# Kernel optimization log

Hardware: AMD Instinct MI355X
Metric: run time of the kernel (lower is better)

Reference implementation:

```python
import jax, jax.numpy as jnp
import numpy as np

N, E, CIN = 50000, 400000, 512
GH, GO, TH, HEADS, COUT = 128, 64, 64, 4, 32
BN_EPS = 1e-5


def setup_inputs() -> dict:
    key = jax.random.key(0)
    ks = jax.random.split(key, 40)
    i = iter(range(40))
    nrm = lambda shape, s=0.05: jax.random.normal(ks[next(i)], shape, jnp.float32) * s
    uni = lambda shape, lo, hi: jax.random.uniform(ks[next(i)], shape, jnp.float32, lo, hi)
    inp = {
        'x': jax.random.normal(ks[next(i)], (N, CIN), jnp.float32),
        'edge_index': jax.random.randint(ks[next(i)], (2, E), 0, N, jnp.int32),
        'edge_weight': uni((E,), 0.0, 1.0),
        # GCN layer 1 + BN1 (eval-mode running stats)
        'W1': nrm((CIN, GH)), 'b1': jnp.zeros((GH,), jnp.float32),
        'g1': uni((GH,), 0.9, 1.1), 'be1': nrm((GH,)), 'm1': nrm((GH,)), 'v1': uni((GH,), 0.5, 1.5),
        # GCN layer 2 + BN2
        'W2': nrm((GH, GO)), 'b2': jnp.zeros((GO,), jnp.float32),
        'g2': uni((GO,), 0.9, 1.1), 'be2': nrm((GO,)), 'm2': nrm((GO,)), 'v2': uni((GO,), 0.5, 1.5),
        # TransformerConv (PyG): lin_q/k/v: GO -> HEADS*TH ; skip: GO -> TH
        'Wq': nrm((GO, HEADS * TH)), 'bq': jnp.zeros((HEADS * TH,), jnp.float32),
        'Wk': nrm((GO, HEADS * TH)), 'bk': jnp.zeros((HEADS * TH,), jnp.float32),
        'Wv': nrm((GO, HEADS * TH)), 'bv': jnp.zeros((HEADS * TH,), jnp.float32),
        'Wskip': nrm((GO, TH)), 'bskip': jnp.zeros((TH,), jnp.float32),
        # BN after transformer
        'gt': uni((TH,), 0.9, 1.1), 'bet': nrm((TH,)), 'mt': nrm((TH,)), 'vt': uni((TH,), 0.5, 1.5),
        # final Linear
        'Wfc': nrm((TH, COUT)), 'bfc': jnp.zeros((COUT,), jnp.float32),
    }
    return inp


def _bn_eval(h, g, b, m, v):
    return (h - m) * (g / jnp.sqrt(v + BN_EPS)) + b


def _gcn_conv(x, src, dst, w, W, b):
    # add self loops with weight 1 (PyG gcn_norm default)
    loop = jnp.arange(N, dtype=src.dtype)
    s = jnp.concatenate([src, loop])
    d = jnp.concatenate([dst, loop])
    w2 = jnp.concatenate([w, jnp.ones((N,), x.dtype)])
    deg = jax.ops.segment_sum(w2, d, num_segments=N)
    dinv = jnp.where(deg > 0, jax.lax.rsqrt(deg), 0.0)
    norm = dinv[s] * w2 * dinv[d]                      # [E+N]
    h = x @ W                                          # [N, F]
    out = jax.ops.segment_sum(norm[:, None] * h[s], d, num_segments=N)
    return out + b


def _transformer_conv(x, src, dst, Wq, bq, Wk, bk, Wv, bv, Wskip, bskip):
    # PyG TransformerConv, concat=False (mean over heads), root_weight=True, no self loops
    q = (x @ Wq + bq).reshape(N, HEADS, TH)
    k = (x @ Wk + bk).reshape(N, HEADS, TH)
    v = (x @ Wv + bv).reshape(N, HEADS, TH)
    score = jnp.einsum('ehd,ehd->eh', q[dst], k[src]) / jnp.sqrt(jnp.float32(TH))  # [E,H]
    smax = jax.ops.segment_max(score, dst, num_segments=N)       # [N,H]
    ex = jnp.exp(score - smax[dst])
    denom = jax.ops.segment_sum(ex, dst, num_segments=N)         # [N,H]
    alpha = ex / (denom[dst] + 1e-16)                            # edge softmax over incoming edges
    agg = jax.ops.segment_sum(alpha[:, :, None] * v[src], dst, num_segments=N)  # [N,H,TH]
    out = agg.mean(axis=1)                                       # concat=False -> head mean
    return out + x @ Wskip + bskip


def reference(x, edge_index, edge_weight,
              W1, b1, g1, be1, m1, v1,
              W2, b2, g2, be2, m2, v2,
              Wq, bq, Wk, bk, Wv, bv, Wskip, bskip,
              gt, bet, mt, vt, Wfc, bfc):
    src, dst = edge_index[0], edge_index[1]
    h = _gcn_conv(x, src, dst, edge_weight, W1, b1)
    h = jax.nn.relu(_bn_eval(h, g1, be1, m1, v1))        # dropout = identity in eval
    h = _gcn_conv(h, src, dst, edge_weight, W2, b2)
    z = jax.nn.relu(_bn_eval(h, g2, be2, m2, v2))
    z = _transformer_conv(z, src, dst, Wq, bq, Wk, bk, Wv, bv, Wskip, bskip)
    z = jax.nn.relu(_bn_eval(z, gt, bet, mt, vt))
    return z @ Wfc + bfc
```

## Files before the change

### kernel.cpp

```cpp
#include <hip/hip_runtime.h>
#include <math.h>

namespace {

constexpr int NN = 50000;
constexpr int EE = 400000;
constexpr int CIN = 512;
constexpr int GH = 128;
constexpr int GO = 64;
constexpr int HEADS = 4;
constexpr int COUT = 32;
constexpr float EPS = 1e-5f;
constexpr int PBLK = (NN + 255) / 256;
constexpr int EDGEB = (EE + 255) / 256;
constexpr int CVTB = (NN * CIN) / 2048;
constexpr int PREPB = 128 + (79872 + 255) / 256;
constexpr int GM = (NN + 63) / 64;

typedef __attribute__((ext_vector_type(8))) _Float16 half8;
typedef __attribute__((ext_vector_type(4))) _Float16 half4;
typedef __attribute__((ext_vector_type(2))) _Float16 half2v;
typedef __attribute__((ext_vector_type(4))) float f32x4;

inline int cdiv(int a, int b) { return (a + b - 1) / b; }

__global__ void k_init0(float* deg, int* cnt) {
  int i = blockIdx.x * blockDim.x + threadIdx.x;
  if (i < NN) { deg[i] = 0.0f; cnt[i] = 0; }
}

__device__ __forceinline__ void prep_body(
    int b, int tid,
    const float* __restrict__ Wq, const float* __restrict__ Wk,
    const float* __restrict__ bq, const float* __restrict__ Wv,
    const float* __restrict__ bv, const float* __restrict__ bsk,
    const float* __restrict__ W1, const float* __restrict__ W2,
    const float* __restrict__ Wsk, const float* __restrict__ Wfc,
    _Float16* __restrict__ Mcp, float* __restrict__ cvec,
    _Float16* __restrict__ Bcatp, float* __restrict__ bcomb,
    _Float16* __restrict__ W1p, _Float16* __restrict__ W2p,
    _Float16* __restrict__ Wfcp) {
  if (b < 64) {
    const int i = b, col = tid, h = col >> 6, j = col & 63;
    float acc = 0.f;
    for (int t = 0; t < 64; ++t)
      acc += Wq[i * 256 + h * 64 + t] * Wk[j * 256 + h * 64 + t];
    Mcp[col * 64 + i] = (_Float16)(0.125f * acc);
    if (i == 0) {
      float c = 0.f;
      for (int t = 0; t < 64; ++t) c += bq[h * 64 + t] * Wk[j * 256 + h * 64 + t];
      cvec[col] = 0.125f * c;
    }
  } else if (b < 128) {
    const int idx = (b - 64) * 256 + tid;
    const int rr = idx >> 6, t = idx & 63;
    const int h = rr >> 6, c = rr & 63;
    Bcatp[(size_t)t * 320 + 64 + rr] = (_Float16)(0.25f * Wv[c * 256 + h * 64 + t]);
    if (b == 64 && tid < 64) {
      float s = 0.f;
#pragma unroll
      for (int h2 = 0; h2 < 4; ++h2) s += bv[h2 * 64 + tid];
      bcomb[tid] = bsk[tid] + 0.25f * s;
    }
  } else {
    const int i = (b - 128) * 256 + tid;
    if (i < 65536) { int k = i >> 7, f = i & 127; W1p[f * 512 + k] = (_Float16)W1[i]; }
    else if (i < 73728) { int rel = i - 65536; int k = rel >> 6, f = rel & 63; W2p[f * 128 + k] = (_Float16)W2[rel]; }
    else if (i < 77824) { int rel = i - 73728; int k = rel >> 6, f = rel & 63; Bcatp[f * 320 + k] = (_Float16)Wsk[rel]; }
    else if (i < 79872) { int rel = i - 77824; int k = rel >> 5, f = rel & 31; Wfcp[f * 64 + k] = (_Float16)Wfc[rel]; }
  }
}

__launch_bounds__(256) __global__
void k_edgeprep(const int* __restrict__ ei, const float* __restrict__ w,
                float* __restrict__ deg, int* __restrict__ cnt,
                int* __restrict__ rank, const float* __restrict__ x,
                _Float16* __restrict__ x16,
                const float* __restrict__ Wq, const float* __restrict__ Wk,
                const float* __restrict__ bq, const float* __restrict__ Wv,
                const float* __restrict__ bv, const float* __restrict__ bsk,
                const float* __restrict__ W1, const float* __restrict__ W2,
                const float* __restrict__ Wsk, const float* __restrict__ Wfc,
                _Float16* __restrict__ Mcp, float* __restrict__ cvec,
                _Float16* __restrict__ Bcatp, float* __restrict__ bcomb,
                _Float16* __restrict__ W1p, _Float16* __restrict__ W2p,
                _Float16* __restrict__ Wfcp) {
  if (blockIdx.x < EDGEB) {
    int e = blockIdx.x * 256 + threadIdx.x;
    if (e < EE) {
      int d = ei[EE + e];
      atomicAdd(&deg[d], w[e]);
      rank[e] = atomicAdd(&cnt[d], 1);
    }
  } else if (blockIdx.x < EDGEB + CVTB) {
    const int base = (blockIdx.x - EDGEB) * 2048 + threadIdx.x * 8;
    const float4 f0 = *reinterpret_cast<const float4*>(x + base);
    const float4 f1 = *reinterpret_cast<const float4*>(x + base + 4);
    half8 o;
    o[0] = (_Float16)f0.x; o[1] = (_Float16)f0.y;
    o[2] = (_Float16)f0.z; o[3] = (_Float16)f0.w;
    o[4] = (_Float16)f1.x; o[5] = (_Float16)f1.y;
    o[6] = (_Float16)f1.z; o[7] = (_Float16)f1.w;
    *reinterpret_cast<half8*>(x16 + base) = o;
  } else {
    prep_body(blockIdx.x - EDGEB - CVTB, threadIdx.x, Wq, Wk, bq, Wv, bv, bsk,
              W1, W2, Wsk, Wfc, Mcp, cvec, Bcatp, bcomb, W1p, W2p, Wfcp);
  }
}

__global__ void k_node1(const int* __restrict__ cnt, float* __restrict__ dinv,
                        int* __restrict__ part, int* __restrict__ bsum,
                        int* __restrict__ blkhist) {
  __shared__ int wsm[4];
  __shared__ int lh[64];
  const int tid = threadIdx.x, lane = tid & 63, wv = tid >> 6;
  const int i = blockIdx.x * 256 + tid;
  if (tid < 64) lh[tid] = 0;
  __syncthreads();
  int v = (i < NN) ? cnt[i] : 0;
  if (i < NN) {
    dinv[i] = rsqrtf(dinv[i] + 1.0f);
    atomicAdd(&lh[min(v, 63)], 1);
  }
  int x = v;
#pragma unroll
  for (int s = 1; s < 64; s <<= 1) {
    int t = __shfl_up(x, s);
    if (lane >= s) x += t;
  }
  if (lane == 63) wsm[wv] = x;
  __syncthreads();
  if (tid == 0) {
    int r = 0;
#pragma unroll
    for (int j = 0; j < 4; ++j) { int t = wsm[j]; wsm[j] = r; r += t; }
    bsum[blockIdx.x] = r;
  }
  __syncthreads();
  if (i < NN) part[i] = wsm[wv] + x - v;
  if (tid < 64) blkhist[blockIdx.x * 64 + tid] = lh[tid];
}

__launch_bounds__(256) __global__
void k_small(int* __restrict__ bsum, int* __restrict__ ro,
             const int* __restrict__ blkhist, int* __restrict__ blkoff) {
  __shared__ int wsm[4];
  __shared__ int qsum[4][64];
  const int tid = threadIdx.x, lane = tid & 63, wv = tid >> 6;
  {
    int v = (tid < PBLK) ? bsum[tid] : 0;
    int x = v;
#pragma unroll
    for (int s = 1; s < 64; s <<= 1) {
      int t = __shfl_up(x, s);
      if (lane >= s) x += t;
    }
    if (lane == 63) wsm[wv] = x;
    __syncthreads();
    if (tid == 0) {
      int r = 0;
#pragma unroll
      for (int j = 0; j < 4; ++j) { int t = wsm[j]; wsm[j] = r; r += t; }
      ro[NN] = r;
    }
    __syncthreads();
    if (tid < PBLK) bsum[tid] = wsm[wv] + x - v;
  }
  const int c0 = wv * 49, c1 = c0 + 49;
  {
    int qs = 0;
    int k = c0;
    for (; k + 4 <= c1; k += 4) {
      int a = blkhist[(k + 0) * 64 + lane];
      int b = blkhist[(k + 1) * 64 + lane];
      int c = blkhist[(k + 2) * 64 + lane];
      int d = blkhist[(k + 3) * 64 + lane];
      qs += (a + b) + (c + d);
    }
    for (; k < c1; ++k) qs += blkhist[k * 64 + lane];
    qsum[wv][lane] = qs;
  }
  __syncthreads();
  int tot = qsum[0][lane] + qsum[1][lane] + qsum[2][lane] + qsum[3][lane];
  int x = tot;
#pragma unroll
  for (int s = 1; s < 64; s <<= 1) {
    int t = __shfl_up(x, s);
    if (lane >= s) x += t;
  }
  int run = x - tot;
  for (int q = 0; q < wv; ++q) run += qsum[q][lane];
  int k = c0;
  for (; k + 4 <= c1; k += 4) {
    int a = blkhist[(k + 0) * 64 + lane];
    int b = blkhist[(k + 1) * 64 + lane];
    int c = blkhist[(k + 2) * 64 + lane];
    int d = blkhist[(k + 3) * 64 + lane];
    blkoff[(k + 0) * 64 + lane] = run;
    blkoff[(k + 1) * 64 + lane] = run + a;
    blkoff[(k + 2) * 64 + lane] = run + a + b;
    blkoff[(k + 3) * 64 + lane] = run + a + b + c;
    run += (a + b) + (c + d);
  }
  for (; k < c1; ++k) {
    int c = blkhist[k * 64 + lane];
    blkoff[k * 64 + lane] = run;
    run += c;
  }
}

__global__ void k_node2(const int* __restrict__ part, const int* __restrict__ bsum,
                        int* __restrict__ ro, const int* __restrict__ cnt,
                        const int* __restrict__ blkoff, int* __restrict__ perm) {
  __shared__ int lcur[64];
  const int tid = threadIdx.x;
  const int i = blockIdx.x * 256 + tid;
  if (tid < 64) lcur[tid] = 0;
  if (i < NN) ro[i] = part[i] + bsum[i >> 8];
  __syncthreads();
  if (i < NN) {
    int b = min(cnt[i], 63);
    int r = atomicAdd(&lcur[b], 1);
    perm[blkoff[blockIdx.x * 64 + b] + r] = i;
  }
}

template <int F, int K, int LDA, bool OUTF32>
__device__ __forceinline__
void hgemm_body(int bid, const _Float16* __restrict__ Av,
                const _Float16* __restrict__ Bp, const float* __restrict__ bias,
                void* __restrict__ Cv, int M) {
  constexpr int MI = 4;
  constexpr int NR = F / 64;
  constexpr int FW = F / 4;
  constexpr int NT = K / 64;

  __shared__ _Float16 Ah[64 * 64];

  const int tid = threadIdx.x;
  const int lane = tid & 63;
  const int wc = tid >> 6;
  const int l15 = lane & 15, lhi = lane >> 4;
  const int m0 = bid * 64;
  const int r = tid >> 2, ch = tid & 3;
  const int gr = min(m0 + r, M - 1);

  f32x4 acc[MI][NR];
#pragma unroll
  for (int mi = 0; mi < MI; ++mi)
#pragma unroll
    for (int ni = 0; ni < NR; ++ni) acc[mi][ni] = (f32x4)0.0f;

  half8 xhA0, xhA1, xhB0, xhB1;
  auto LOADA = [&](int kk) {
    const half8* src = reinterpret_cast<const half8*>(
        Av + (size_t)gr * LDA + kk + ch * 16);
    xhA0 = src[0]; xhA1 = src[1];
  };
  auto LOADB = [&](int kk) {
    const half8* src = reinterpret_cast<const half8*>(
        Av + (size_t)gr * LDA + kk + ch * 16);
    xhB0 = src[0]; xhB1 = src[1];
  };
  const int sbase = r * 128 + ch * 32;
  const int ssw = (r & 7) << 4;
  auto STOREA = [&]() {
    *reinterpret_cast<half8*>((char*)Ah + (sbase ^ ssw)) = xhA0;
    *reinterpret_cast<half8*>((char*)Ah + ((sbase + 16) ^ ssw)) = xhA1;
  };
  auto STOREB = [&]() {
    *reinterpret_cast<half8*>((char*)Ah + (sbase ^ ssw)) = xhB0;
    *reinterpret_cast<half8*>((char*)Ah + ((sbase + 16) ^ ssw)) = xhB1;
  };

  LOADA(0);
  if constexpr (NT > 1) LOADB(64);

#pragma unroll
  for (int t = 0; t < NT; ++t) {
    if ((t & 1) == 0) STOREA(); else STOREB();
    __syncthreads();
    if ((t & 1) == 0) {
      if (t + 2 < NT) LOADA((t + 2) * 64);
    } else {
      if (t + 2 < NT) LOADB((t + 2) * 64);
    }
    const int k0 = t * 64;
#pragma unroll
    for (int ks = 0; ks < 2; ++ks) {
      half8 ah[MI];
#pragma unroll
      for (int mi = 0; mi < MI; ++mi) {
        const int row = mi * 16 + l15;
        const int off = (row * 128 + (ks * 32 + lhi * 8) * 2) ^ ((row & 7) << 4);
        ah[mi] = *reinterpret_cast<const half8*>((const char*)Ah + off);
      }
#pragma unroll
      for (int ni = 0; ni < NR; ++ni) {
        const int col = wc * FW + ni * 16 + l15;
        const half8 bf = *reinterpret_cast<const half8*>(
            Bp + (size_t)col * K + k0 + ks * 32 + lhi * 8);
#pragma unroll
        for (int mi = 0; mi < MI; ++mi)
          acc[mi][ni] = __builtin_amdgcn_mfma_f32_16x16x32_f16(ah[mi], bf, acc[mi][ni], 0, 0, 0);
      }
    }
    __syncthreads();
  }

#pragma unroll
  for (int ni = 0; ni < NR; ++ni) {
    const int col = wc * FW + ni * 16 + l15;
    const float bvv = bias ? bias[col] : 0.0f;
#pragma unroll
    for (int mi = 0; mi < MI; ++mi) {
#pragma unroll
      for (int rr = 0; rr < 4; ++rr) {
        const int orow = m0 + mi * 16 + lhi * 4 + rr;
        if (orow < M) {
          float val = acc[mi][ni][rr] + bvv;
          if (OUTF32)
            ((float*)Cv)[(size_t)orow * F + col] = val;
          else
            ((_Float16*)Cv)[(size_t)orow * F + col] = (_Float16)val;
        }
      }
    }
  }
}

template <int F, int K, int LDA, bool OUTF32>
__launch_bounds__(256) __global__
void hgemm(const _Float16* __restrict__ Av, const _Float16* __restrict__ Bp,
           const float* __restrict__ bias, void* __restrict__ Cv, int M) {
  hgemm_body<F, K, LDA, OUTF32>(blockIdx.x, Av, Bp, bias, Cv, M);
}

__launch_bounds__(256) __global__
void k_fillgemm1(const int* __restrict__ ei, const float* __restrict__ w,
                 const float* __restrict__ dinv, const int* __restrict__ ro,
                 const int* __restrict__ rank, int2* __restrict__ csrp,
                 const _Float16* __restrict__ x16,
                 const _Float16* __restrict__ W1p, _Float16* __restrict__ h1f,
                 int M) {
  if (blockIdx.x < GM) {
    hgemm_body<128, 512, 512, false>(blockIdx.x, x16, W1p, nullptr, h1f, M);
  } else {
    int e = (blockIdx.x - GM) * 256 + threadIdx.x;
    if (e < EE) {
      int s = ei[e], d = ei[EE + e];
      int p = ro[d] + rank[e];
      int2 pk;
      pk.x = s;
      pk.y = __float_as_int(dinv[s] * w[e] * dinv[d]);
      csrp[p] = pk;
    }
  }
}

__launch_bounds__(256) __global__
void k_aggfc(const _Float16* __restrict__ zu, const _Float16* __restrict__ Bcatp,
             const float* __restrict__ bcomb, const _Float16* __restrict__ Wfcp,
             const float* __restrict__ bfc, float* __restrict__ out, int M,
             const float* __restrict__ gt, const float* __restrict__ bet,
             const float* __restrict__ mt, const float* __restrict__ vt) {
  __shared__ _Float16 Ah[64 * 64];
  __shared__ _Float16 Gs[64 * 64];

  const int tid = threadIdx.x;
  const int lane = tid & 63;
  const int wid = tid >> 6;
  const int l15 = lane & 15, lhi = lane >> 4;
  const int m0 = blockIdx.x * 64;
  const int r = tid >> 2, ch = tid & 3;
  const int gr = min(m0 + r, M - 1);

  f32x4 acc[4];
#pragma unroll
  for (int mi = 0; mi < 4; ++mi) acc[mi] = (f32x4)0.0f;

  half8 xhA0, xhA1, xhB0, xhB1;
  auto LOADA = [&](int kk) {
    const half8* src = reinterpret_cast<const half8*>(
        zu + (size_t)gr * 320 + kk + ch * 16);
    xhA0 = src[0]; xhA1 = src[1];
  };
  auto LOADB = [&](int kk) {
    const half8* src = reinterpret_cast<const half8*>(
        zu + (size_t)gr * 320 + kk + ch * 16);
    xhB0 = src[0]; xhB1 = src[1];
  };
  const int sbase = r * 128 + ch * 32;
  const int ssw = (r & 7) << 4;
  auto STOREA = [&]() {
    *reinterpret_cast<half8*>((char*)Ah + (sbase ^ ssw)) = xhA0;
    *reinterpret_cast<half8*>((char*)Ah + ((sbase + 16) ^ ssw)) = xhA1;
  };
  auto STOREB = [&]() {
    *reinterpret_cast<half8*>((char*)Ah + (sbase ^ ssw)) = xhB0;
    *reinterpret_cast<half8*>((char*)Ah + ((sbase + 16) ^ ssw)) = xhB1;
  };

  LOADA(0);
  LOADB(64);
#pragma unroll
  for (int t = 0; t < 5; ++t) {
    if ((t & 1) == 0) STOREA(); else STOREB();
    __syncthreads();
    if ((t & 1) == 0) {
      if (t + 2 < 5) LOADA((t + 2) * 64);
    } else {
      if (t + 2 < 5) LOADB((t + 2) * 64);
    }
    const int k0 = t * 64;
#pragma unroll
    for (int ks = 0; ks < 2; ++ks) {
      half8 ah[4];
#pragma unroll
      for (int mi = 0; mi < 4; ++mi) {
        const int row = mi * 16 + l15;
        const int off = (row * 128 + (ks * 32 + lhi * 8) * 2) ^ ((row & 7) << 4);
        ah[mi] = *reinterpret_cast<const half8*>((const char*)Ah + off);
      }
      const int col = wid * 16 + l15;
      const half8 bf = *reinterpret_cast<const half8*>(
          Bcatp + (size_t)col * 320 + k0 + ks * 32 + lhi * 8);
#pragma unroll
      for (int mi = 0; mi < 4; ++mi)
        acc[mi] = __builtin_amdgcn_mfma_f32_16x16x32_f16(ah[mi], bf, acc[mi], 0, 0, 0);
    }
    __syncthreads();
  }

  {
    const int col = wid * 16 + l15;
    const float bns = gt[col] * rsqrtf(vt[col] + EPS);
    const float bnb = bet[col], bnm = mt[col], bco = bcomb[col];
#pragma unroll
    for (int mi = 0; mi < 4; ++mi) {
#pragma unroll
      for (int rr = 0; rr < 4; ++rr) {
        const int row = mi * 16 + lhi * 4 + rr;
        float val = acc[mi][rr] + bco;
        val = (val - bnm) * bns + bnb;
        val = val > 0.f ? val : 0.f;
        const int boff = (row * 128 + col * 2) ^ ((row & 7) << 4);
        *reinterpret_cast<_Float16*>((char*)Gs + boff) = (_Float16)val;
      }
    }
  }
  __syncthreads();

  f32x4 acc2[2];
#pragma unroll
  for (int ni = 0; ni < 2; ++ni) acc2[ni] = (f32x4)0.0f;
#pragma unroll
  for (int ks = 0; ks < 2; ++ks) {
    const int row = wid * 16 + l15;
    const int off = (row * 128 + (ks * 32 + lhi * 8) * 2) ^ ((row & 7) << 4);
    const half8 ag = *reinterpret_cast<const half8*>((const char*)Gs + off);
#pragma unroll
    for (int ni = 0; ni < 2; ++ni) {
      const int col = ni * 16 + l15;
      const half8 bf = *reinterpret_cast<const half8*>(
          Wfcp + (size_t)col * 64 + ks * 32 + lhi * 8);
      acc2[ni] = __builtin_amdgcn_mfma_f32_16x16x32_f16(ag, bf, acc2[ni], 0, 0, 0);
    }
  }
#pragma unroll
  for (int ni = 0; ni < 2; ++ni) {
    const int col = ni * 16 + l15;
#pragma unroll
    for (int rr = 0; rr < 4; ++rr) {
      const int orow = m0 + wid * 16 + lhi * 4 + rr;
      if (orow < M) out[(size_t)orow * COUT + col] = acc2[ni][rr] + bfc[col];
    }
  }
}

__launch_bounds__(256) __global__
void k_gcn128(const int* __restrict__ ro, const int2* __restrict__ csrp,
              const int* __restrict__ perm,
              const _Float16* __restrict__ h, const float* __restrict__ dinv,
              const float* __restrict__ bias, const float* __restrict__ g,
              const float* __restrict__ be, const float* __restrict__ m,
              const float* __restrict__ v, _Float16* __restrict__ out) {
  const int idx = blockIdx.x * 4 + (threadIdx.x >> 6);
  const int lane = threadIdx.x & 63;
  if (idx >= NN) return;
  const int wid = perm[idx];
  const float di = dinv[wid];
  const float di2 = di * di;
  const int p0 = ro[wid], p1 = ro[wid + 1];

  half2v sv = *reinterpret_cast<const half2v*>(h + (size_t)wid * 128 + lane * 2);
  float2 a[4];
  a[0] = make_float2((float)sv[0] * di2, (float)sv[1] * di2);
  a[1] = make_float2(0.f, 0.f);
  a[2] = make_float2(0.f, 0.f);
  a[3] = make_float2(0.f, 0.f);
  int p = p0;
  for (; p + 8 <= p1; p += 8) {
    int2 pk[8];
#pragma unroll
    for (int j = 0; j < 8; ++j) pk[j] = csrp[p + j];
    half2v hv[8];
#pragma unroll
    for (int j = 0; j < 8; ++j)
      hv[j] = *reinterpret_cast<const half2v*>(h + (size_t)pk[j].x * 128 + lane * 2);
#pragma unroll
    for (int j = 0; j < 8; ++j) {
      float w = __int_as_float(pk[j].y);
      a[j & 3].x += w * (float)hv[j][0];
      a[j & 3].y += w * (float)hv[j][1];
    }
  }
  for (; p + 4 <= p1; p += 4) {
    int2 pk[4];
#pragma unroll
    for (int j = 0; j < 4; ++j) pk[j] = csrp[p + j];
    half2v hv[4];
#pragma unroll
    for (int j = 0; j < 4; ++j)
      hv[j] = *reinterpret_cast<const half2v*>(h + (size_t)pk[j].x * 128 + lane * 2);
#pragma unroll
    for (int j = 0; j < 4; ++j) {
      float w = __int_as_float(pk[j].y);
      a[j].x += w * (float)hv[j][0];
      a[j].y += w * (float)hv[j][1];
    }
  }
  for (; p < p1; ++p) {
    int2 pk = csrp[p];
    float w = __int_as_float(pk.y);
    half2v hv = *reinterpret_cast<const half2v*>(h + (size_t)pk.x * 128 + lane * 2);
    a[1].x += w * (float)hv[0]; a[1].y += w * (float)hv[1];
  }
  float ax = (a[0].x + a[1].x) + (a[2].x + a[3].x);
  float ay = (a[0].y + a[1].y) + (a[2].y + a[3].y);
  float2 gg = reinterpret_cast<const float2*>(g)[lane];
  float2 bb = reinterpret_cast<const float2*>(be)[lane];
  float2 mm = reinterpret_cast<const float2*>(m)[lane];
  float2 vv = reinterpret_cast<const float2*>(v)[lane];
  float2 bi = reinterpret_cast<const float2*>(bias)[lane];
  float s0 = gg.x * rsqrtf(vv.x + EPS);
  float s1 = gg.y * rsqrtf(vv.y + EPS);
  float y0 = (ax + bi.x - mm.x) * s0 + bb.x;
  float y1 = (ay + bi.y - mm.y) * s1 + bb.y;
  half2v o;
  o[0] = (_Float16)(y0 > 0.f ? y0 : 0.f);
  o[1] = (_Float16)(y1 > 0.f ? y1 : 0.f);
  *reinterpret_cast<half2v*>(out + (size_t)wid * 128 + lane * 2) = o;
}

__launch_bounds__(256) __global__
void k_gcn64(const int* __restrict__ ro, const int2* __restrict__ csrp,
             const int* __restrict__ perm,
             const _Float16* __restrict__ h, const float* __restrict__ dinv,
             const float* __restrict__ bias, const float* __restrict__ g,
             const float* __restrict__ be, const float* __restrict__ m,
             const float* __restrict__ v, _Float16* __restrict__ zu) {
  const int idx = blockIdx.x * 4 + (threadIdx.x >> 6);
  const int lane = threadIdx.x & 63;
  if (idx >= NN) return;
  const int wid = perm[idx];
  const float di = dinv[wid];
  const float di2 = di * di;
  const int p0 = ro[wid], p1 = ro[wid + 1];

  float a[4];
  a[0] = (float)h[(size_t)wid * 64 + lane] * di2;
  a[1] = 0.f; a[2] = 0.f; a[3] = 0.f;
  int p = p0;
  for (; p + 8 <= p1; p += 8) {
    int2 pk[8];
#pragma unroll
    for (int j = 0; j < 8; ++j) pk[j] = csrp[p + j];
    float hv[8];
#pragma unroll
    for (int j = 0; j < 8; ++j) hv[j] = (float)h[(size_t)pk[j].x * 64 + lane];
#pragma unroll
    for (int j = 0; j < 8; ++j) a[j & 3] += __int_as_float(pk[j].y) * hv[j];
  }
  for (; p + 4 <= p1; p += 4) {
    int2 pk[4];
#pragma unroll
    for (int j = 0; j < 4; ++j) pk[j] = csrp[p + j];
    float hv[4];
#pragma unroll
    for (int j = 0; j < 4; ++j) hv[j] = (float)h[(size_t)pk[j].x * 64 + lane];
#pragma unroll
    for (int j = 0; j < 4; ++j) a[j] += __int_as_float(pk[j].y) * hv[j];
  }
  for (; p < p1; ++p) {
    int2 pk = csrp[p];
    a[1] += __int_as_float(pk.y) * (float)h[(size_t)pk.x * 64 + lane];
  }
  float av = (a[0] + a[1]) + (a[2] + a[3]);
  float sc = g[lane] * rsqrtf(v[lane] + EPS);
  float y = (av + bias[lane] - m[lane]) * sc + be[lane];
  zu[(size_t)wid * 320 + lane] = (_Float16)(y > 0.f ? y : 0.f);
}

__launch_bounds__(256) __global__
void k_attn(const int* __restrict__ ro, const int2* __restrict__ csrp,
            const int* __restrict__ perm, _Float16* zu,
            const _Float16* __restrict__ qpp) {
  const int wave = blockIdx.x * 4 + (threadIdx.x >> 6);
  const int lane = threadIdx.x & 63;
  const int g = lane >> 4;
  const int t = lane & 15;
  const bool bit3 = (t & 8) != 0, bit2 = (t & 4) != 0;

  const int idx = wave * 4 + g;
  const bool valid = idx < NN;
  const int dst = perm[valid ? idx : 0];

  float4 q[4];
#pragma unroll
  for (int h = 0; h < 4; ++h) {
    half4 qh = *reinterpret_cast<const half4*>(qpp + (size_t)dst * 256 + h * 64 + t * 4);
    q[h] = make_float4((float)qh[0], (float)qh[1], (float)qh[2], (float)qh[3]);
  }

  float4 ua[4];
  float den[4];
#pragma unroll
  for (int h = 0; h < 4; ++h) {
    ua[h] = make_float4(0.f, 0.f, 0.f, 0.f);
    den[h] = 0.f;
  }

  int p = valid ? ro[dst] : 0;
  const int pend = valid ? ro[dst + 1] : 0;

  auto reduce4 = [&](float pa0, float pa1, float pa2, float pa3,
                     float& o0, float& o1, float& o2, float& o3) {
    float send1 = bit3 ? pa0 : pa2;
    float recv1 = __shfl_xor(send1, 8);
    float a0 = (bit3 ? pa2 : pa0) + recv1;
    float send2 = bit3 ? pa1 : pa3;
    float recv2 = __shfl_xor(send2, 8);
    float a1 = (bit3 ? pa3 : pa1) + recv2;
    float send3 = bit2 ? a0 : a1;
    float recv3 = __shfl_xor(send3, 4);
    float b = (bit2 ? a1 : a0) + recv3;
    b += __shfl_xor(b, 2);
    b += __shfl_xor(b, 1);
    float r4 = __shfl_xor(b, 4);
    float r8 = __shfl_xor(b, 8);
    float r84 = __shfl_xor(r4, 8);
    o0 = bit3 ? (bit2 ? r84 : r8) : (bit2 ? r4 : b);
    o1 = bit3 ? (bit2 ? r8 : r84) : (bit2 ? b : r4);
    o2 = bit3 ? (bit2 ? r4 : b) : (bit2 ? r84 : r8);
    o3 = bit3 ? (bit2 ? b : r4) : (bit2 ? r8 : r84);
  };

  int sA = csrp[min(p, EE - 1)].x;
  int sB = csrp[min(p + 1, EE - 1)].x;
  half4 znA = *reinterpret_cast<const half4*>(zu + (size_t)sA * 320 + t * 4);
  half4 znB = *reinterpret_cast<const half4*>(zu + (size_t)sB * 320 + t * 4);

  while (__ballot(p < pend)) {
    const bool actA = p < pend;
    const bool actB = (p + 1) < pend;
    const float4 zvA = make_float4((float)znA[0], (float)znA[1], (float)znA[2], (float)znA[3]);
    const float4 zvB = make_float4((float)znB[0], (float)znB[1], (float)znB[2], (float)znB[3]);
    sA = csrp[min(p + 2, EE - 1)].x;
    sB = csrp[min(p + 3, EE - 1)].x;
    znA = *reinterpret_cast<const half4*>(zu + (size_t)sA * 320 + t * 4);
    znB = *reinterpret_cast<const half4*>(zu + (size_t)sB * 320 + t * 4);

    float pA0 = q[0].x * zvA.x + q[0].y * zvA.y + q[0].z * zvA.z + q[0].w * zvA.w;
    float pA1 = q[1].x * zvA.x + q[1].y * zvA.y + q[1].z * zvA.z + q[1].w * zvA.w;
    float pA2 = q[2].x * zvA.x + q[2].y * zvA.y + q[2].z * zvA.z + q[2].w * zvA.w;
    float pA3 = q[3].x * zvA.x + q[3].y * zvA.y + q[3].z * zvA.z + q[3].w * zvA.w;
    float pB0 = q[0].x * zvB.x + q[0].y * zvB.y + q[0].z * zvB.z + q[0].w * zvB.w;
    float pB1 = q[1].x * zvB.x + q[1].y * zvB.y + q[1].z * zvB.z + q[1].w * zvB.w;
    float pB2 = q[2].x * zvB.x + q[2].y * zvB.y + q[2].z * zvB.z + q[2].w * zvB.w;
    float pB3 = q[3].x * zvB.x + q[3].y * zvB.y + q[3].z * zvB.z + q[3].w * zvB.w;

    float sA0, sA1, sA2, sA3, sB0, sB1, sB2, sB3;
    reduce4(pA0, pA1, pA2, pA3, sA0, sA1, sA2, sA3);
    reduce4(pB0, pB1, pB2, pB3, sB0, sB1, sB2, sB3);

    float eA0 = actA ? __expf(fminf(sA0, 60.f)) : 0.f;
    float eA1 = actA ? __expf(fminf(sA1, 60.f)) : 0.f;
    float eA2 = actA ? __expf(fminf(sA2, 60.f)) : 0.f;
    float eA3 = actA ? __expf(fminf(sA3, 60.f)) : 0.f;
    float eB0 = actB ? __expf(fminf(sB0, 60.f)) : 0.f;
    float eB1 = actB ? __expf(fminf(sB1, 60.f)) : 0.f;
    float eB2 = actB ? __expf(fminf(sB2, 60.f)) : 0.f;
    float eB3 = actB ? __expf(fminf(sB3, 60.f)) : 0.f;

    den[0] += eA0 + eB0; den[1] += eA1 + eB1;
    den[2] += eA2 + eB2; den[3] += eA3 + eB3;
    ua[0].x += eA0 * zvA.x + eB0 * zvB.x; ua[0].y += eA0 * zvA.y + eB0 * zvB.y;
    ua[0].z += eA0 * zvA.z + eB0 * zvB.z; ua[0].w += eA0 * zvA.w + eB0 * zvB.w;
    ua[1].x += eA1 * zvA.x + eB1 * zvB.x; ua[1].y += eA1 * zvA.y + eB1 * zvB.y;
    ua[1].z += eA1 * zvA.z + eB1 * zvB.z; ua[1].w += eA1 * zvA.w + eB1 * zvB.w;
    ua[2].x += eA2 * zvA.x + eB2 * zvB.x; ua[2].y += eA2 * zvA.y + eB2 * zvB.y;
    ua[2].z += eA2 * zvA.z + eB2 * zvB.z; ua[2].w += eA2 * zvA.w + eB2 * zvB.w;
    ua[3].x += eA3 * zvA.x + eB3 * zvB.x; ua[3].y += eA3 * zvA.y + eB3 * zvB.y;
    ua[3].z += eA3 * zvA.z + eB3 * zvB.z; ua[3].w += eA3 * zvA.w + eB3 * zvB.w;
    p += 2;
  }

  if (valid) {
#pragma unroll
    for (int h = 0; h < 4; ++h) {
      float inv = 1.0f / (den[h] + 1e-16f);
      half4 o;
      o[0] = (_Float16)(ua[h].x * inv);
      o[1] = (_Float16)(ua[h].y * inv);
      o[2] = (_Float16)(ua[h].z * inv);
      o[3] = (_Float16)(ua[h].w * inv);
      *reinterpret_cast<half4*>(zu + (size_t)dst * 320 + 64 + h * 64 + t * 4) = o;
    }
  }
}

}

extern "C" void kernel_launch(void* const* d_in, const int* in_sizes, int n_in,
                              void* d_out, int out_size, void* d_ws, size_t ws_size,
                              hipStream_t stream) {
  const float* x   = (const float*)d_in[0];
  const int*   ei  = (const int*)d_in[1];
  const float* ew  = (const float*)d_in[2];
  const float* W1  = (const float*)d_in[3];
  const float* b1  = (const float*)d_in[4];
  const float* g1  = (const float*)d_in[5];
  const float* be1 = (const float*)d_in[6];
  const float* m1  = (const float*)d_in[7];
  const float* v1  = (const float*)d_in[8];
  const float* W2  = (const float*)d_in[9];
  const float* b2  = (const float*)d_in[10];
  const float* g2  = (const float*)d_in[11];
  const float* be2 = (const float*)d_in[12];
  const float* m2  = (const float*)d_in[13];
  const float* v2  = (const float*)d_in[14];
  const float* Wq  = (const float*)d_in[15];
  const float* bq  = (const float*)d_in[16];
  const float* Wk  = (const float*)d_in[17];
  const float* Wv  = (const float*)d_in[19];
  const float* bv  = (const float*)d_in[20];
  const float* Wsk = (const float*)d_in[21];
  const float* bsk = (const float*)d_in[22];
  const float* gt  = (const float*)d_in[23];
  const float* bet = (const float*)d_in[24];
  const float* mt  = (const float*)d_in[25];
  const float* vt  = (const float*)d_in[26];
  const float* Wfc = (const float*)d_in[27];
  const float* bfc = (const float*)d_in[28];

  constexpr int NP = 50048;
  float* ws = (float*)d_ws;
  float* dinv    = ws;
  int*   cnt     = (int*)(dinv + NP);
  int*   rank    = cnt + NP;
  int*   ro      = rank + EE;
  int*   perm    = ro + NP;
  int*   part    = perm + NP;
  int*   bsum    = part + NP;
  int2*  csrp    = (int2*)(bsum + 256);
  int*   blkhist = (int*)(csrp + EE);
  int*   blkoff  = blkhist + PBLK * 64;
  float* cvec    = (float*)(blkoff + PBLK * 64 + 64);
  float* bcomb   = cvec + 256;
  _Float16* Mcp   = (_Float16*)(bcomb + 64);
  _Float16* Bcatp = Mcp + 256 * 64;
  _Float16* W1p   = Bcatp + 64 * 320;
  _Float16* W2p   = W1p + 128 * 512;
  _Float16* Wfcp  = W2p + 64 * 128;
  _Float16* x16   = Wfcp + 32 * 64;
  _Float16* h1f   = x16 + (size_t)NP * 512;
  _Float16* a1f   = h1f + (size_t)NP * 128;
  _Float16* h2f   = a1f + (size_t)NP * 128;
  _Float16* zuf   = h2f + (size_t)NP * 64;
  _Float16* qppf  = zuf + (size_t)NP * 320;

  const int tb = 256;

  k_init0<<<cdiv(NN, tb), tb, 0, stream>>>(dinv, cnt);
  k_edgeprep<<<EDGEB + CVTB + PREPB, 256, 0, stream>>>(
      ei, ew, dinv, cnt, rank, x, x16, Wq, Wk, bq, Wv, bv, bsk, W1, W2, Wsk, Wfc,
      Mcp, cvec, Bcatp, bcomb, W1p, W2p, Wfcp);
  k_node1<<<PBLK, 256, 0, stream>>>(cnt, dinv, part, bsum, blkhist);
  k_small<<<1, 256, 0, stream>>>(bsum, ro, blkhist, blkoff);
  k_node2<<<PBLK, 256, 0, stream>>>(part, bsum, ro, cnt, blkoff, perm);

  k_fillgemm1<<<GM + EDGEB, 256, 0, stream>>>(ei, ew, dinv, ro, rank, csrp,
                                              x16, W1p, h1f, NN);

  k_gcn128<<<cdiv(NN, 4), 256, 0, stream>>>(ro, csrp, perm, h1f, dinv,
                                            b1, g1, be1, m1, v1, a1f);
  hgemm<64, 128, 128, false><<<GM, 256, 0, stream>>>(a1f, W2p, nullptr, h2f, NN);
  k_gcn64<<<cdiv(NN, 4), 256, 0, stream>>>(ro, csrp, perm, h2f, dinv,
                                           b2, g2, be2, m2, v2, zuf);

  hgemm<256, 64, 320, false><<<GM, 256, 0, stream>>>(zuf, Mcp, cvec, qppf, NN);
  k_attn<<<cdiv(NN, 16), 256, 0, stream>>>(ro, csrp, perm, zuf, qppf);

  k_aggfc<<<GM, 256, 0, stream>>>(zuf, Bcatp, bcomb, Wfcp, bfc, (float*)d_out, NN,
                                  gt, bet, mt, vt);
}
```

Before: 239.3 us.

## Fuse fp32-to-fp16 conversion into GEMM1 and compute degree from CSR

Removes the separate x→fp16 conversion pass: the first GEMM now loads fp32 x directly and converts it while staging into shared memory. This avoids writing and rereading the 51 MB fp16 copy, at the cost of doubled A-operand load bytes inside the GEMM. The atomic float degree accumulation is replaced by a new per-node kernel that sums CSR edge weights. The CSR now stores raw weights, so the GCN kernels gather dinv[src] per edge and scale by dinv[dst] at the end, adding an extra gather per edge.

```diff
diff --git a/kernel.cpp b/kernel.cpp
--- a/kernel.cpp
+++ b/kernel.cpp
@@ -13,7 +13,6 @@
 constexpr float EPS = 1e-5f;
 constexpr int PBLK = (NN + 255) / 256;
 constexpr int EDGEB = (EE + 255) / 256;
-constexpr int CVTB = (NN * CIN) / 2048;
 constexpr int PREPB = 128 + (79872 + 255) / 256;
 constexpr int GM = (NN + 63) / 64;
 
@@ -24,9 +23,9 @@
 
 inline int cdiv(int a, int b) { return (a + b - 1) / b; }
 
-__global__ void k_init0(float* deg, int* cnt) {
+__global__ void k_init0(int* cnt) {
   int i = blockIdx.x * blockDim.x + threadIdx.x;
-  if (i < NN) { deg[i] = 0.0f; cnt[i] = 0; }
+  if (i < NN) cnt[i] = 0;
 }
 
 __device__ __forceinline__ void prep_body(
@@ -72,10 +71,8 @@
 }
 
 __launch_bounds__(256) __global__
-void k_edgeprep(const int* __restrict__ ei, const float* __restrict__ w,
-                float* __restrict__ deg, int* __restrict__ cnt,
-                int* __restrict__ rank, const float* __restrict__ x,
-                _Float16* __restrict__ x16,
+void k_edgeprep(const int* __restrict__ ei, int* __restrict__ cnt,
+                int* __restrict__ rank,
                 const float* __restrict__ Wq, const float* __restrict__ Wk,
                 const float* __restrict__ bq, const float* __restrict__ Wv,
                 const float* __restrict__ bv, const float* __restrict__ bsk,
@@ -89,28 +86,16 @@
     int e = blockIdx.x * 256 + threadIdx.x;
     if (e < EE) {
       int d = ei[EE + e];
-      atomicAdd(&deg[d], w[e]);
       rank[e] = atomicAdd(&cnt[d], 1);
     }
-  } else if (blockIdx.x < EDGEB + CVTB) {
-    const int base = (blockIdx.x - EDGEB) * 2048 + threadIdx.x * 8;
-    const float4 f0 = *reinterpret_cast<const float4*>(x + base);
-    const float4 f1 = *reinterpret_cast<const float4*>(x + base + 4);
-    half8 o;
-    o[0] = (_Float16)f0.x; o[1] = (_Float16)f0.y;
-    o[2] = (_Float16)f0.z; o[3] = (_Float16)f0.w;
-    o[4] = (_Float16)f1.x; o[5] = (_Float16)f1.y;
-    o[6] = (_Float16)f1.z; o[7] = (_Float16)f1.w;
-    *reinterpret_cast<half8*>(x16 + base) = o;
   } else {
-    prep_body(blockIdx.x - EDGEB - CVTB, threadIdx.x, Wq, Wk, bq, Wv, bv, bsk,
+    prep_body(blockIdx.x - EDGEB, threadIdx.x, Wq, Wk, bq, Wv, bv, bsk,
               W1, W2, Wsk, Wfc, Mcp, cvec, Bcatp, bcomb, W1p, W2p, Wfcp);
   }
 }
 
-__global__ void k_node1(const int* __restrict__ cnt, float* __restrict__ dinv,
-                        int* __restrict__ part, int* __restrict__ bsum,
-                        int* __restrict__ blkhist) {
+__global__ void k_node1(const int* __restrict__ cnt, int* __restrict__ part,
+                        int* __restrict__ bsum, int* __restrict__ blkhist) {
   __shared__ int wsm[4];
   __shared__ int lh[64];
   const int tid = threadIdx.x, lane = tid & 63, wv = tid >> 6;
@@ -118,10 +103,7 @@
   if (tid < 64) lh[tid] = 0;
   __syncthreads();
   int v = (i < NN) ? cnt[i] : 0;
-  if (i < NN) {
-    dinv[i] = rsqrtf(dinv[i] + 1.0f);
-    atomicAdd(&lh[min(v, 63)], 1);
-  }
+  if (i < NN) atomicAdd(&lh[min(v, 63)], 1);
   int x = v;
 #pragma unroll
   for (int s = 1; s < 64; s <<= 1) {
@@ -225,9 +207,9 @@
   }
 }
 
-template <int F, int K, int LDA, bool OUTF32>
+template <int F, int K, int LDA, bool AF32C, bool OUTF32>
 __device__ __forceinline__
-void hgemm_body(int bid, const _Float16* __restrict__ Av,
+void hgemm_body(int bid, const void* __restrict__ Av,
                 const _Float16* __restrict__ Bp, const float* __restrict__ bias,
                 void* __restrict__ Cv, int M) {
   constexpr int MI = 4;
@@ -251,26 +233,69 @@
 #pragma unroll
     for (int ni = 0; ni < NR; ++ni) acc[mi][ni] = (f32x4)0.0f;
 
+  float xfA[16], xfB[16];
   half8 xhA0, xhA1, xhB0, xhB1;
+
   auto LOADA = [&](int kk) {
-    const half8* src = reinterpret_cast<const half8*>(
-        Av + (size_t)gr * LDA + kk + ch * 16);
-    xhA0 = src[0]; xhA1 = src[1];
+    if constexpr (AF32C) {
+      const float4* src = reinterpret_cast<const float4*>(
+          (const float*)Av + (size_t)gr * LDA + kk + ch * 16);
+      float4 f0 = src[0], f1 = src[1], f2 = src[2], f3 = src[3];
+      xfA[0] = f0.x; xfA[1] = f0.y; xfA[2] = f0.z; xfA[3] = f0.w;
+      xfA[4] = f1.x; xfA[5] = f1.y; xfA[6] = f1.z; xfA[7] = f1.w;
+      xfA[8] = f2.x; xfA[9] = f2.y; xfA[10] = f2.z; xfA[11] = f2.w;
+      xfA[12] = f3.x; xfA[13] = f3.y; xfA[14] = f3.z; xfA[15] = f3.w;
+    } else {
+      const half8* src = reinterpret_cast<const half8*>(
+          (const _Float16*)Av + (size_t)gr * LDA + kk + ch * 16);
+      xhA0 = src[0]; xhA1 = src[1];
+    }
   };
   auto LOADB = [&](int kk) {
-    const half8* src = reinterpret_cast<const half8*>(
-        Av + (size_t)gr * LDA + kk + ch * 16);
-    xhB0 = src[0]; xhB1 = src[1];
+    if constexpr (AF32C) {
+      const float4* src = reinterpret_cast<const float4*>(
+          (const float*)Av + (size_t)gr * LDA + kk + ch * 16);
+      float4 f0 = src[0], f1 = src[1], f2 = src[2], f3 = src[3];
+      xfB[0] = f0.x; xfB[1] = f0.y; xfB[2] = f0.z; xfB[3] = f0.w;
+      xfB[4] = f1.x; xfB[5] = f1.y; xfB[6] = f1.z; xfB[7] = f1.w;
+      xfB[8] = f2.x; xfB[9] = f2.y; xfB[10] = f2.z; xfB[11] = f2.w;
+      xfB[12] = f3.x; xfB[13] = f3.y; xfB[14] = f3.z; xfB[15] = f3.w;
+    } else {
+      const half8* src = reinterpret_cast<const half8*>(
+          (const _Float16*)Av + (size_t)gr * LDA + kk + ch * 16);
+      xhB0 = src[0]; xhB1 = src[1];
+    }
   };
+
   const int sbase = r * 128 + ch * 32;
   const int ssw = (r & 7) << 4;
   auto STOREA = [&]() {
-    *reinterpret_cast<half8*>((char*)Ah + (sbase ^ ssw)) = xhA0;
-    *reinterpret_cast<half8*>((char*)Ah + ((sbase + 16) ^ ssw)) = xhA1;
+    if constexpr (AF32C) {
+      half8 v0, v1;
+#pragma unroll
+      for (int i = 0; i < 8; ++i) v0[i] = (_Float16)xfA[i];
+#pragma unroll
+      for (int i = 0; i < 8; ++i) v1[i] = (_Float16)xfA[8 + i];
+      *reinterpret_cast<half8*>((char*)Ah + (sbase ^ ssw)) = v0;
+      *reinterpret_cast<half8*>((char*)Ah + ((sbase + 16) ^ ssw)) = v1;
+    } else {
+      *reinterpret_cast<half8*>((char*)Ah + (sbase ^ ssw)) = xhA0;
+      *reinterpret_cast<half8*>((char*)Ah + ((sbase + 16) ^ ssw)) = xhA1;
+    }
   };
   auto STOREB = [&]() {
-    *reinterpret_cast<half8*>((char*)Ah + (sbase ^ ssw)) = xhB0;
-    *reinterpret_cast<half8*>((char*)Ah + ((sbase + 16) ^ ssw)) = xhB1;
+    if constexpr (AF32C) {
+      half8 v0, v1;
+#pragma unroll
+      for (int i = 0; i < 8; ++i) v0[i] = (_Float16)xfB[i];
+#pragma unroll
+      for (int i = 0; i < 8; ++i) v1[i] = (_Float16)xfB[8 + i];
+      *reinterpret_cast<half8*>((char*)Ah + (sbase ^ ssw)) = v0;
+      *reinterpret_cast<half8*>((char*)Ah + ((sbase + 16) ^ ssw)) = v1;
+    } else {
+      *reinterpret_cast<half8*>((char*)Ah + (sbase ^ ssw)) = xhB0;
+      *reinterpret_cast<half8*>((char*)Ah + ((sbase + 16) ^ ssw)) = xhB1;
+    }
   };
 
   LOADA(0);
@@ -329,33 +354,48 @@
   }
 }
 
-template <int F, int K, int LDA, bool OUTF32>
+template <int F, int K, int LDA, bool AF32C, bool OUTF32>
 __launch_bounds__(256) __global__
-void hgemm(const _Float16* __restrict__ Av, const _Float16* __restrict__ Bp,
+void hgemm(const void* __restrict__ Av, const _Float16* __restrict__ Bp,
            const float* __restrict__ bias, void* __restrict__ Cv, int M) {
-  hgemm_body<F, K, LDA, OUTF32>(blockIdx.x, Av, Bp, bias, Cv, M);
+  hgemm_body<F, K, LDA, AF32C, OUTF32>(blockIdx.x, Av, Bp, bias, Cv, M);
 }
 
 __launch_bounds__(256) __global__
 void k_fillgemm1(const int* __restrict__ ei, const float* __restrict__ w,
-                 const float* __restrict__ dinv, const int* __restrict__ ro,
-                 const int* __restrict__ rank, int2* __restrict__ csrp,
-                 const _Float16* __restrict__ x16,
+                 const int* __restrict__ ro, const int* __restrict__ rank,
+                 int2* __restrict__ csrp, const float* __restrict__ x,
                  const _Float16* __restrict__ W1p, _Float16* __restrict__ h1f,
                  int M) {
   if (blockIdx.x < GM) {
-    hgemm_body<128, 512, 512, false>(blockIdx.x, x16, W1p, nullptr, h1f, M);
+    hgemm_body<128, 512, 512, true, false>(blockIdx.x, x, W1p, nullptr, h1f, M);
   } else {
     int e = (blockIdx.x - GM) * 256 + threadIdx.x;
     if (e < EE) {
-      int s = ei[e], d = ei[EE + e];
+      int d = ei[EE + e];
       int p = ro[d] + rank[e];
       int2 pk;
-      pk.x = s;
-      pk.y = __float_as_int(dinv[s] * w[e] * dinv[d]);
+      pk.x = ei[e];
+      pk.y = __float_as_int(w[e]);
       csrp[p] = pk;
     }
   }
+}
+
+__global__ void k_deg(const int* __restrict__ ro, const int2* __restrict__ csrp,
+                      float* __restrict__ dinv) {
+  int d = blockIdx.x * 256 + threadIdx.x;
+  if (d >= NN) return;
+  int p = ro[d];
+  const int p1 = ro[d + 1];
+  float s0 = 0.f, s1 = 0.f, s2 = 0.f, s3 = 0.f;
+  for (; p + 4 <= p1; p += 4) {
+    int2 a = csrp[p], b = csrp[p + 1], c = csrp[p + 2], e = csrp[p + 3];
+    s0 += __int_as_float(a.y); s1 += __int_as_float(b.y);
+    s2 += __int_as_float(c.y); s3 += __int_as_float(e.y);
+  }
+  for (; p < p1; ++p) s0 += __int_as_float(csrp[p].y);
+  dinv[d] = rsqrtf(1.0f + (s0 + s1) + (s2 + s3));
 }
 
 __launch_bounds__(256) __global__
@@ -480,22 +520,21 @@
 
 __launch_bounds__(256) __global__
 void k_gcn128(const int* __restrict__ ro, const int2* __restrict__ csrp,
-              const int* __restrict__ perm,
-              const _Float16* __restrict__ h, const float* __restrict__ dinv,
-              const float* __restrict__ bias, const float* __restrict__ g,
-              const float* __restrict__ be, const float* __restrict__ m,
-              const float* __restrict__ v, _Float16* __restrict__ out) {
+              const int* __restrict__ perm, const _Float16* __restrict__ h,
+              const float* __restrict__ dinv, const float* __restrict__ bias,
+              const float* __restrict__ g, const float* __restrict__ be,
+              const float* __restrict__ m, const float* __restrict__ v,
+              _Float16* __restrict__ out) {
   const int idx = blockIdx.x * 4 + (threadIdx.x >> 6);
   const int lane = threadIdx.x & 63;
   if (idx >= NN) return;
   const int wid = perm[idx];
   const float di = dinv[wid];
-  const float di2 = di * di;
   const int p0 = ro[wid], p1 = ro[wid + 1];
 
   half2v sv = *reinterpret_cast<const half2v*>(h + (size_t)wid * 128 + lane * 2);
   float2 a[4];
-  a[0] = make_float2((float)sv[0] * di2, (float)sv[1] * di2);
+  a[0] = make_float2((float)sv[0] * di, (float)sv[1] * di);
   a[1] = make_float2(0.f, 0.f);
   a[2] = make_float2(0.f, 0.f);
   a[3] = make_float2(0.f, 0.f);
@@ -504,40 +543,46 @@
     int2 pk[8];
 #pragma unroll
     for (int j = 0; j < 8; ++j) pk[j] = csrp[p + j];
+    float ds[8];
+#pragma unroll
+    for (int j = 0; j < 8; ++j) ds[j] = dinv[pk[j].x];
     half2v hv[8];
 #pragma unroll
     for (int j = 0; j < 8; ++j)
       hv[j] = *reinterpret_cast<const half2v*>(h + (size_t)pk[j].x * 128 + lane * 2);
 #pragma unroll
     for (int j = 0; j < 8; ++j) {
-      float w = __int_as_float(pk[j].y);
-      a[j & 3].x += w * (float)hv[j][0];
-      a[j & 3].y += w * (float)hv[j][1];
+      float c = ds[j] * __int_as_float(pk[j].y);
+      a[j & 3].x += c * (float)hv[j][0];
+      a[j & 3].y += c * (float)hv[j][1];
     }
   }
   for (; p + 4 <= p1; p += 4) {
     int2 pk[4];
 #pragma unroll
     for (int j = 0; j < 4; ++j) pk[j] = csrp[p + j];
+    float ds[4];
+#pragma unroll
+    for (int j = 0; j < 4; ++j) ds[j] = dinv[pk[j].x];
     half2v hv[4];
 #pragma unroll
     for (int j = 0; j < 4; ++j)
       hv[j] = *reinterpret_cast<const half2v*>(h + (size_t)pk[j].x * 128 + lane * 2);
 #pragma unroll
     for (int j = 0; j < 4; ++j) {
-      float w = __int_as_float(pk[j].y);
-      a[j].x += w * (float)hv[j][0];
-      a[j].y += w * (float)hv[j][1];
+      float c = ds[j] * __int_as_float(pk[j].y);
+      a[j].x += c * (float)hv[j][0];
+      a[j].y += c * (float)hv[j][1];
     }
   }
   for (; p < p1; ++p) {
     int2 pk = csrp[p];
-    float w = __int_as_float(pk.y);
+    float c = dinv[pk.x] * __int_as_float(pk.y);
     half2v hv = *reinterpret_cast<const half2v*>(h + (size_t)pk.x * 128 + lane * 2);
-    a[1].x += w * (float)hv[0]; a[1].y += w * (float)hv[1];
-  }
-  float ax = (a[0].x + a[1].x) + (a[2].x + a[3].x);
-  float ay = (a[0].y + a[1].y) + (a[2].y + a[3].y);
+    a[1].x += c * (float)hv[0]; a[1].y += c * (float)hv[1];
+  }
+  float ax = ((a[0].x + a[1].x) + (a[2].x + a[3].x)) * di;
+  float ay = ((a[0].y + a[1].y) + (a[2].y + a[3].y)) * di;
   float2 gg = reinterpret_cast<const float2*>(g)[lane];
   float2 bb = reinterpret_cast<const float2*>(be)[lane];
   float2 mm = reinterpret_cast<const float2*>(m)[lane];
@@ -555,48 +600,53 @@
 
 __launch_bounds__(256) __global__
 void k_gcn64(const int* __restrict__ ro, const int2* __restrict__ csrp,
-             const int* __restrict__ perm,
-             const _Float16* __restrict__ h, const float* __restrict__ dinv,
-             const float* __restrict__ bias, const float* __restrict__ g,
-             const float* __restrict__ be, const float* __restrict__ m,
-             const float* __restrict__ v, _Float16* __restrict__ zu) {
+             const int* __restrict__ perm, const _Float16* __restrict__ h,
+             const float* __restrict__ dinv, const float* __restrict__ bias,
+             const float* __restrict__ g, const float* __restrict__ be,
+             const float* __restrict__ m, const float* __restrict__ v,
+             _Float16* __restrict__ zu) {
   const int idx = blockIdx.x * 4 + (threadIdx.x >> 6);
   const int lane = threadIdx.x & 63;
   if (idx >= NN) return;
   const int wid = perm[idx];
   const float di = dinv[wid];
-  const float di2 = di * di;
   const int p0 = ro[wid], p1 = ro[wid + 1];
 
   float a[4];
-  a[0] = (float)h[(size_t)wid * 64 + lane] * di2;
+  a[0] = (float)h[(size_t)wid * 64 + lane] * di;
   a[1] = 0.f; a[2] = 0.f; a[3] = 0.f;
   int p = p0;
   for (; p + 8 <= p1; p += 8) {
     int2 pk[8];
 #pragma unroll
     for (int j = 0; j < 8; ++j) pk[j] = csrp[p + j];
+    float ds[8];
+#pragma unroll
+    for (int j = 0; j < 8; ++j) ds[j] = dinv[pk[j].x];
     float hv[8];
 #pragma unroll
     for (int j = 0; j < 8; ++j) hv[j] = (float)h[(size_t)pk[j].x * 64 + lane];
 #pragma unroll
-    for (int j = 0; j < 8; ++j) a[j & 3] += __int_as_float(pk[j].y) * hv[j];
+    for (int j = 0; j < 8; ++j) a[j & 3] += ds[j] * __int_as_float(pk[j].y) * hv[j];
   }
   for (; p + 4 <= p1; p += 4) {
     int2 pk[4];
 #pragma unroll
     for (int j = 0; j < 4; ++j) pk[j] = csrp[p + j];
+    float ds[4];
+#pragma unroll
+    for (int j = 0; j < 4; ++j) ds[j] = dinv[pk[j].x];
     float hv[4];
 #pragma unroll
     for (int j = 0; j < 4; ++j) hv[j] = (float)h[(size_t)pk[j].x * 64 + lane];
 #pragma unroll
-    for (int j = 0; j < 4; ++j) a[j] += __int_as_float(pk[j].y) * hv[j];
+    for (int j = 0; j < 4; ++j) a[j] += ds[j] * __int_as_float(pk[j].y) * hv[j];
   }
   for (; p < p1; ++p) {
     int2 pk = csrp[p];
-    a[1] += __int_as_float(pk.y) * (float)h[(size_t)pk.x * 64 + lane];
-  }
-  float av = (a[0] + a[1]) + (a[2] + a[3]);
+    a[1] += dinv[pk.x] * __int_as_float(pk.y) * (float)h[(size_t)pk.x * 64 + lane];
+  }
+  float av = ((a[0] + a[1]) + (a[2] + a[3])) * di;
   float sc = g[lane] * rsqrtf(v[lane] + EPS);
   float y = (av + bias[lane] - m[lane]) * sc + be[lane];
   zu[(size_t)wid * 320 + lane] = (_Float16)(y > 0.f ? y : 0.f);
@@ -773,8 +823,7 @@
   _Float16* W1p   = Bcatp + 64 * 320;
   _Float16* W2p   = W1p + 128 * 512;
   _Float16* Wfcp  = W2p + 64 * 128;
-  _Float16* x16   = Wfcp + 32 * 64;
-  _Float16* h1f   = x16 + (size_t)NP * 512;
+  _Float16* h1f   = Wfcp + 32 * 64;
   _Float16* a1f   = h1f + (size_t)NP * 128;
   _Float16* h2f   = a1f + (size_t)NP * 128;
   _Float16* zuf   = h2f + (size_t)NP * 64;
@@ -782,24 +831,25 @@
 
   const int tb = 256;
 
-  k_init0<<<cdiv(NN, tb), tb, 0, stream>>>(dinv, cnt);
-  k_edgeprep<<<EDGEB + CVTB + PREPB, 256, 0, stream>>>(
-      ei, ew, dinv, cnt, rank, x, x16, Wq, Wk, bq, Wv, bv, bsk, W1, W2, Wsk, Wfc,
+  k_init0<<<cdiv(NN, tb), tb, 0, stream>>>(cnt);
+  k_edgeprep<<<EDGEB + PREPB, 256, 0, stream>>>(
+      ei, cnt, rank, Wq, Wk, bq, Wv, bv, bsk, W1, W2, Wsk, Wfc,
       Mcp, cvec, Bcatp, bcomb, W1p, W2p, Wfcp);
-  k_node1<<<PBLK, 256, 0, stream>>>(cnt, dinv, part, bsum, blkhist);
+  k_node1<<<PBLK, 256, 0, stream>>>(cnt, part, bsum, blkhist);
   k_small<<<1, 256, 0, stream>>>(bsum, ro, blkhist, blkoff);
   k_node2<<<PBLK, 256, 0, stream>>>(part, bsum, ro, cnt, blkoff, perm);
 
-  k_fillgemm1<<<GM + EDGEB, 256, 0, stream>>>(ei, ew, dinv, ro, rank, csrp,
-                                              x16, W1p, h1f, NN);
+  k_fillgemm1<<<GM + EDGEB, 256, 0, stream>>>(ei, ew, ro, rank, csrp,
+                                              x, W1p, h1f, NN);
+  k_deg<<<cdiv(NN, tb), tb, 0, stream>>>(ro, csrp, dinv);
 
   k_gcn128<<<cdiv(NN, 4), 256, 0, stream>>>(ro, csrp, perm, h1f, dinv,
                                             b1, g1, be1, m1, v1, a1f);
-  hgemm<64, 128, 128, false><<<GM, 256, 0, stream>>>(a1f, W2p, nullptr, h2f, NN);
+  hgemm<64, 128, 128, false, false><<<GM, 256, 0, stream>>>(a1f, W2p, nullptr, h2f, NN);
   k_gcn64<<<cdiv(NN, 4), 256, 0, stream>>>(ro, csrp, perm, h2f, dinv,
                                            b2, g2, be2, m2, v2, zuf);
 
-  hgemm<256, 64, 320, false><<<GM, 256, 0, stream>>>(zuf, Mcp, cvec, qppf, NN);
+  hgemm<256, 64, 320, false, false><<<GM, 256, 0, stream>>>(zuf, Mcp, cvec, qppf, NN);
   k_attn<<<cdiv(NN, 16), 256, 0, stream>>>(ro, csrp, perm, zuf, qppf);
 
   k_aggfc<<<GM, 256, 0, stream>>>(zuf, Bcatp, bcomb, Wfcp, bfc, (float*)d_out, NN,
```

After: 208.4 us. 12.9% less time.
